# Kernel optimization log

Hardware: AMD Instinct MI355X
Metric: run time of the kernel (lower is better)

Reference implementation:

```python
import jax, jax.numpy as jnp
import numpy as np

TEMP = 0.07
K = 16  # n_hard_negatives
NEG = jnp.float32(-1e30)


def setup_inputs() -> dict:
    key = jax.random.key(0)
    k1, k2 = jax.random.split(key)
    B, D = 8192, 512
    emb = jax.random.normal(k1, (B, D), dtype=jnp.float32)
    emb = emb / jnp.linalg.norm(emb, axis=1, keepdims=True)  # module expects L2-normalized
    labels = jax.random.randint(k2, (B,), 0, 2048, dtype=jnp.int64)
    return {"embeddings": emb, "labels": labels}


def _masked_topk(sim, valid, k):
    # sim: [B,B] float, valid: [B,B] bool -> (top values [B,k], per-slot validity [B,k])
    masked = jnp.where(valid, sim, NEG)
    top = jax.lax.top_k(masked, k)[0]
    count = jnp.sum(valid, axis=1)
    kmask = jnp.arange(k)[None, :] < jnp.minimum(count, k)[:, None]
    return top, kmask


def reference(embeddings, labels):
    B = embeddings.shape[0]
    sim = embeddings @ embeddings.T                      # [B,B]
    same = labels[:, None] == labels[None, :]
    eye = jnp.eye(B, dtype=bool)
    pos_mask = same & ~eye                               # positives exclude self
    neg_mask = ~same                                     # diagonal is 'same', so self excluded

    pos_count = jnp.sum(pos_mask, axis=1)
    neg_count = jnp.sum(neg_mask, axis=1)
    row_valid = (pos_count > 0) & (neg_count > 0)

    # semi-hard: negatives with sim < min positive sim
    pos_min = jnp.min(jnp.where(pos_mask, sim, -NEG), axis=1)     # [B]
    semi = neg_mask & (sim < pos_min[:, None])
    has_semi = jnp.any(semi, axis=1)

    top_semi, m_semi = _masked_topk(sim, semi, K)
    top_all, m_all = _masked_topk(sim, neg_mask, K)
    top = jnp.where(has_semi[:, None], top_semi, top_all)         # [B,K]
    kmask = jnp.where(has_semi[:, None], m_semi, m_all)           # [B,K]

    pos_sim = jnp.sum(jnp.where(pos_mask, sim, 0.0), axis=1) / jnp.maximum(pos_count, 1) / TEMP

    # masked logsumexp over the (variable-length) top-k hard negatives
    scaled = jnp.where(kmask, top / TEMP, NEG)
    m = jnp.max(scaled, axis=1)
    sum_exp = jnp.sum(jnp.where(kmask, jnp.exp(scaled - m[:, None]), 0.0), axis=1)
    lse = m + jnp.log(jnp.maximum(sum_exp, 1e-30))

    loss_i = -pos_sim + lse
    n_valid = jnp.sum(row_valid)
    return jnp.sum(jnp.where(row_valid, loss_i, 0.0)) / jnp.maximum(n_valid, 1)
```

## Files before the change

### kernel.cpp

```cpp
#include <hip/hip_runtime.h>
#include <stdint.h>
#include <stddef.h>


#define TEMPV 0.07f
#define NEGV -1e30f

typedef short v8s __attribute__((ext_vector_type(8)));
typedef float v4f __attribute__((ext_vector_type(4)));

__device__ __forceinline__ short f2bf(float f) {
  unsigned u = __float_as_uint(f);
  unsigned r = (u + 0x7fffu + ((u >> 16) & 1u)) >> 16;
  return (short)r;
}
__device__ __forceinline__ float bf2f(short s) {
  return __uint_as_float(((unsigned)(unsigned short)s) << 16);
}

__device__ __forceinline__ void gload16(const void* g, void* l) {
  __builtin_amdgcn_global_load_lds((const __attribute__((address_space(1))) unsigned*)g,
                                   (__attribute__((address_space(3))) unsigned*)l, 16, 0, 0);
}

struct SNet { unsigned char a[64]; unsigned char b[64]; int n; };
constexpr SNet mknet16() {
  SNet t{}; t.n = 0;
  for (int p = 1; p < 16; p <<= 1)
    for (int k = p; k >= 1; k >>= 1)
      for (int j = k % p; j + k < 16; j += 2 * k)
        for (int i = 0; i < k; ++i) {
          int x = i + j, y = i + j + k;
          if (y < 16 && (x / (2 * p)) == (y / (2 * p))) {
            t.a[t.n] = (unsigned char)x; t.b[t.n] = (unsigned char)y; ++t.n;
          }
        }
  return t;
}
constexpr SNet NET16 = mknet16();
constexpr int NETN = NET16.n;

__device__ __forceinline__ void sort16d(float (&V)[16]) {
#pragma unroll
  for (int c = 0; c < NETN; ++c) {
    const int x = NET16.a[c], y = NET16.b[c];
    float hi = fmaxf(V[x], V[y]);
    float lo = fminf(V[x], V[y]);
    V[x] = hi; V[y] = lo;
  }
}

__device__ __forceinline__ void clean16d(float (&V)[16]) {
#pragma unroll
  for (int s = 8; s >= 1; s >>= 1) {
#pragma unroll
    for (int i = 0; i < 16; ++i) {
      if ((i & s) == 0) {
        float hi = fmaxf(V[i], V[i + s]);
        float lo = fminf(V[i], V[i + s]);
        V[i] = hi; V[i + s] = lo;
      }
    }
  }
}

__device__ __forceinline__ void mergeld(float (&R)[16], const float (&M)[16]) {
#pragma unroll
  for (int i = 0; i < 8; ++i) {
    float a = fmaxf(M[i], R[15 - i]);
    float b = fmaxf(M[15 - i], R[i]);
    R[i] = a; R[15 - i] = b;
  }
  clean16d(R);
}

__device__ __forceinline__ void xmerge16(float (&M)[16], int mask) {
#pragma unroll
  for (int i = 0; i < 8; ++i) {
    float pa = __shfl_xor(M[15 - i], mask);
    float pb = __shfl_xor(M[i], mask);
    M[i] = fmaxf(M[i], pa);
    M[15 - i] = fmaxf(M[15 - i], pb);
  }
  clean16d(M);
}

__device__ __forceinline__ void ins16(float (&L)[16], float v) {
#pragma unroll
  for (int k = 0; k < 15; ++k) {
    float lo = fminf(v, L[k + 1]);
    float hi = fmaxf(v, L[k + 1]);
    L[k] = lo;
    v = hi;
  }
  L[15] = v;
}

__global__ __launch_bounds__(256) void kconvh(const float* __restrict__ emb,
                                              short* __restrict__ emb16,
                                              const int* __restrict__ lab,
                                              int* __restrict__ hist,
                                              int* __restrict__ start,
                                              int* __restrict__ rows,
                                              float* lsum, int* nval, int* fbcnt) {
  __shared__ int h[2048];
  __shared__ int part[256];
  int t = threadIdx.x;
  if (blockIdx.x < 4096) {
    int i = (blockIdx.x * 256 + t) * 4;
    float4 v = *(const float4*)(emb + i);
    short4 s;
    s.x = f2bf(v.x); s.y = f2bf(v.y); s.z = f2bf(v.z); s.w = f2bf(v.w);
    *(short4*)(emb16 + i) = s;
    if (blockIdx.x == 0 && t == 0) { *lsum = 0.f; *nval = 0; *fbcnt = 0; }
    return;
  }
#pragma unroll
  for (int k = 0; k < 8; ++k) h[t * 8 + k] = 0;
  __syncthreads();
  for (int i = t; i < 8192; i += 256) atomicAdd(&h[lab[i]], 1);
  __syncthreads();
  int v[8], loc[8], s = 0;
#pragma unroll
  for (int k = 0; k < 8; ++k) v[k] = h[t * 8 + k];
#pragma unroll
  for (int k = 0; k < 8; ++k) { loc[k] = s; s += v[k]; }
  part[t] = s;
  __syncthreads();
  for (int off = 1; off < 256; off <<= 1) {
    int x = (t >= off) ? part[t - off] : 0;
    __syncthreads();
    part[t] += x;
    __syncthreads();
  }
  int base = (t > 0) ? part[t - 1] : 0;
#pragma unroll
  for (int k = 0; k < 8; ++k) {
    hist[t * 8 + k] = v[k];
    start[t * 8 + k] = base + loc[k];
  }
  __syncthreads();
#pragma unroll
  for (int k = 0; k < 8; ++k) h[t * 8 + k] = base + loc[k];
  __syncthreads();
  for (int i = t; i < 8192; i += 256) {
    int p = atomicAdd(&h[lab[i]], 1);
    rows[p] = i;
  }
}

__global__ __launch_bounds__(256) void kpos2(const short* __restrict__ emb16,
                                             const int* __restrict__ lab,
                                             const int* __restrict__ hist,
                                             const int* __restrict__ start,
                                             const int* __restrict__ rows,
                                             float* __restrict__ pmin,
                                             float* __restrict__ pterm,
                                             int* __restrict__ valid) {
  int t = threadIdx.x;
  int wv = t >> 6, lane = t & 63;
  int i = blockIdx.x * 4 + wv;
  int li = lab[i];
  int s0 = start[li], c = hist[li];
  float ei[8];
  v8s e = *(const v8s*)(emb16 + (size_t)i * 512 + lane * 8);
#pragma unroll
  for (int k = 0; k < 8; ++k) ei[k] = bf2f(e[k]);
  float smin = 1e30f, ssum = 0.f;
  for (int k = 0; k < c; ++k) {
    int j = rows[s0 + k];
    if (j == i) continue;
    v8s f = *(const v8s*)(emb16 + (size_t)j * 512 + lane * 8);
    float s = 0.f;
#pragma unroll
    for (int q = 0; q < 8; ++q) s += ei[q] * bf2f(f[q]);
#pragma unroll
    for (int off = 32; off; off >>= 1) s += __shfl_xor(s, off);
    smin = fminf(smin, s);
    ssum += s;
  }
  if (lane == 0) {
    int pc = c - 1, nc = 8192 - c;
    pmin[i] = smin;
    pterm[i] = ssum / (float)(pc > 0 ? pc : 1) / TEMPV;
    valid[i] = (pc > 0 && nc > 0) ? 1 : 0;
  }
}

__global__ __launch_bounds__(256, 2) void kgemm(const short* __restrict__ emb16,
                                                const int* __restrict__ lab,
                                                const float* __restrict__ pminA,
                                                float* __restrict__ Lsemi) {
  __shared__ __align__(16) short Cg[2][128][64];

  int t = threadIdx.x;
  int bid = blockIdx.x;
  int rb = bid >> 3, cb = bid & 7;
  int rowbase = rb * 64;
  int colblock = cb * 1024;

  int wv = t >> 6, l = t & 63;
  int l15 = l & 15, l4 = l >> 4;

  int myrow = rowbase + wv * 16 + l15;
  int rlab = lab[myrow];
  float pm = pminA[myrow];

  v8s brow[8][2];
#pragma unroll
  for (int kst = 0; kst < 8; ++kst)
#pragma unroll
    for (int h = 0; h < 2; ++h)
      brow[kst][h] =
          *(const v8s*)(emb16 + (size_t)myrow * 512 + kst * 64 + h * 32 + l4 * 8);

  float RS[16];
#pragma unroll
  for (int k = 0; k < 16; ++k) RS[k] = NEGV;

  v4f acc[8];
#pragma unroll
  for (int mi = 0; mi < 8; ++mi) acc[mi] = (v4f)0.f;

#pragma unroll
  for (int q = 0; q < 4; ++q) {
    int e = q * 256 + t;
    int col = e >> 3, ch = e & 7;
    gload16(emb16 + ((size_t)(colblock + col) * 512 + ((ch ^ (col & 7)) * 8)),
            &Cg[0][col][ch * 8]);
  }
  asm volatile("s_waitcnt vmcnt(0)" ::: "memory");
  __builtin_amdgcn_s_barrier();

  const int apos0 = (l4 ^ (l15 & 7)) * 8;

  for (int ct = 0; ct < 8; ++ct) {
#pragma unroll
    for (int kst = 0; kst < 8; ++kst) {
      const int cur = kst & 1;
      v8s a0[8], a1[8];
#pragma unroll
      for (int mi = 0; mi < 8; ++mi)
        a0[mi] = *(const v8s*)&Cg[cur][mi * 16 + l15][apos0];
#pragma unroll
      for (int mi = 0; mi < 8; ++mi)
        a1[mi] = *(const v8s*)&Cg[cur][mi * 16 + l15][apos0 ^ 32];
      if (!(ct == 7 && kst == 7)) {
        const int nct = (kst == 7) ? ct + 1 : ct;
        const int nk = ((kst + 1) & 7) * 64;
#pragma unroll
        for (int q = 0; q < 4; ++q) {
          int e = q * 256 + t;
          int col = e >> 3, ch = e & 7;
          gload16(emb16 + ((size_t)(colblock + nct * 128 + col) * 512 + nk +
                           ((ch ^ (col & 7)) * 8)),
                  &Cg[cur ^ 1][col][ch * 8]);
        }
      }
      __builtin_amdgcn_s_setprio(1);
#pragma unroll
      for (int mi = 0; mi < 8; ++mi)
        acc[mi] = __builtin_amdgcn_mfma_f32_16x16x32_bf16(a0[mi], brow[kst][0],
                                                          acc[mi], 0, 0, 0);
#pragma unroll
      for (int mi = 0; mi < 8; ++mi)
        acc[mi] = __builtin_amdgcn_mfma_f32_16x16x32_bf16(a1[mi], brow[kst][1],
                                                          acc[mi], 0, 0, 0);
      __builtin_amdgcn_s_setprio(0);
      if (kst == 7) {
        const int mycolbase = colblock + ct * 128;
#pragma unroll
        for (int c = 0; c < 2; ++c) {
          int lc[4][4];
#pragma unroll
          for (int mm = 0; mm < 4; ++mm) {
            int4 q = *(const int4*)&lab[mycolbase + (c * 4 + mm) * 16 + l4 * 4];
            lc[mm][0] = q.x; lc[mm][1] = q.y; lc[mm][2] = q.z; lc[mm][3] = q.w;
          }
          float S[16];
#pragma unroll
          for (int j = 0; j < 16; ++j) {
            const int mi = c * 4 + (j >> 2), r = j & 3;
            float v = acc[mi][r];
            bool keep = (lc[j >> 2][r] != rlab) && (v < pm);
            S[j] = keep ? v : NEGV;
          }
          sort16d(S);
          mergeld(RS, S);
        }
#pragma unroll
        for (int mi = 0; mi < 8; ++mi) acc[mi] = (v4f)0.f;
      }
      asm volatile("s_waitcnt vmcnt(0)" ::: "memory");
      __builtin_amdgcn_s_barrier();
    }
  }

  xmerge16(RS, 16);
  xmerge16(RS, 32);
  if (l4 == 0) {
    size_t o = ((size_t)cb * 8192 + myrow) * 16;
#pragma unroll
    for (int k = 0; k < 4; ++k)
      *(float4*)&Lsemi[o + k * 4] =
          make_float4(RS[k * 4], RS[k * 4 + 1], RS[k * 4 + 2], RS[k * 4 + 3]);
  }
}

__global__ __launch_bounds__(256) void kfin(const float* __restrict__ Lsemi,
                                            const float* __restrict__ pterm,
                                            const int* __restrict__ valid,
                                            float* lsum, int* nval,
                                            int* fbcnt, int* fbrows) {
  int i = blockIdx.x * 256 + threadIdx.x;
  float S[16], M[16];
#pragma unroll
  for (int k = 0; k < 16; ++k) S[k] = Lsemi[(size_t)i * 16 + k];
  for (int c = 1; c < 8; ++c) {
    size_t o = ((size_t)c * 8192 + i) * 16;
#pragma unroll
    for (int k = 0; k < 16; ++k) M[k] = Lsemi[o + k];
    mergeld(S, M);
  }
  int vd = valid[i];
  bool hs = S[0] > -1e29f;
  float li = 0.f;
  if (vd && !hs) {
    int idx = atomicAdd(fbcnt, 1);
    fbrows[idx] = i;
  } else if (vd) {
    float m = S[0] / TEMPV;
    float se = 0.f;
#pragma unroll
    for (int k = 0; k < 16; ++k)
      if (S[k] > -1e29f) se += expf(S[k] / TEMPV - m);
    li = m + logf(se) - pterm[i];
  }
#pragma unroll
  for (int off = 32; off; off >>= 1) {
    li += __shfl_xor(li, off);
    vd += __shfl_xor(vd, off);
  }
  __shared__ float rsd[4];
  __shared__ int rid[4];
  int wv = threadIdx.x >> 6;
  if ((threadIdx.x & 63) == 0) { rsd[wv] = li; rid[wv] = vd; }
  __syncthreads();
  if (threadIdx.x == 0) {
    atomicAdd(lsum, rsd[0] + rsd[1] + rsd[2] + rsd[3]);
    atomicAdd(nval, rid[0] + rid[1] + rid[2] + rid[3]);
  }
}

__global__ __launch_bounds__(256) void kfallA(const short* __restrict__ emb16,
                                              const int* __restrict__ lab,
                                              const int* __restrict__ fbcnt,
                                              const int* __restrict__ fbrows,
                                              float* __restrict__ fbpart) {
  int nfb = *fbcnt;
  if (nfb > 2048) nfb = 2048;
  int nunits = nfb * 32;
  __shared__ short remb[512];
  __shared__ float sims[256];
  int t = threadIdx.x;
  for (int u = blockIdx.x; u < nunits; u += gridDim.x) {
    int f = u >> 5, j = u & 31;
    int row = fbrows[f];
    int rl = lab[row];
    __syncthreads();
    if (t < 64) *(v8s*)&remb[t * 8] = *(const v8s*)(emb16 + (size_t)row * 512 + t * 8);
    __syncthreads();
    int c = j * 256 + t;
    float sz[8];
#pragma unroll
    for (int z = 0; z < 8; ++z) sz[z] = 0.f;
#pragma unroll 4
    for (int q = 0; q < 64; ++q) {
      v8s e = *(const v8s*)(emb16 + (size_t)c * 512 + q * 8);
      v8s r = *(const v8s*)&remb[q * 8];
#pragma unroll
      for (int z = 0; z < 8; ++z) sz[z] += bf2f(e[z]) * bf2f(r[z]);
    }
    float s = ((sz[0] + sz[1]) + (sz[2] + sz[3])) + ((sz[4] + sz[5]) + (sz[6] + sz[7]));
    sims[t] = (lab[c] != rl) ? s : NEGV;
    __syncthreads();
    if (t < 64) {
      float M[16];
#pragma unroll
      for (int k = 0; k < 16; ++k) M[k] = NEGV;
      M[0] = sims[t]; M[1] = sims[64 + t]; M[2] = sims[128 + t]; M[3] = sims[192 + t];
      sort16d(M);
      xmerge16(M, 1); xmerge16(M, 2); xmerge16(M, 4);
      xmerge16(M, 8); xmerge16(M, 16); xmerge16(M, 32);
      if (t == 0) {
#pragma unroll
        for (int k = 0; k < 16; ++k) fbpart[(size_t)(f * 32 + j) * 16 + k] = M[k];
      }
    }
  }
}

__global__ __launch_bounds__(256) void kout(const short* __restrict__ emb16,
                                            const int* __restrict__ lab,
                                            const int* __restrict__ fbcnt,
                                            const int* __restrict__ fbrows,
                                            const float* __restrict__ fbpart,
                                            const float* __restrict__ pterm,
                                            const float* lsum, const int* nval,
                                            float* out) {
  __shared__ float fsum[256];
  int t = threadIdx.x;
  int nfb = *fbcnt;
  float acc = 0.f;
  for (int f = t; f < nfb; f += 256) {
    int row = fbrows[f];
    float R[16];
    if (f < 2048) {
#pragma unroll
      for (int k = 0; k < 16; ++k) R[k] = fbpart[(size_t)(f * 32) * 16 + k];
      for (int j = 1; j < 32; ++j) {
        float M[16];
#pragma unroll
        for (int k = 0; k < 16; ++k) M[k] = fbpart[(size_t)(f * 32 + j) * 16 + k];
        mergeld(R, M);
      }
    } else {
      int rl = lab[row];
      float L[16];
#pragma unroll
      for (int k = 0; k < 16; ++k) L[k] = NEGV;
      for (int c = 0; c < 8192; ++c) {
        if (lab[c] == rl) continue;
        float s = 0.f;
        for (int q = 0; q < 64; ++q) {
          v8s e = *(const v8s*)(emb16 + (size_t)c * 512 + q * 8);
          v8s r = *(const v8s*)(emb16 + (size_t)row * 512 + q * 8);
#pragma unroll
          for (int z = 0; z < 8; ++z) s += bf2f(e[z]) * bf2f(r[z]);
        }
        if (s > L[0]) ins16(L, s);
      }
#pragma unroll
      for (int k = 0; k < 16; ++k) R[k] = L[15 - k];
    }
    float m = R[0] / TEMPV;
    float se = 0.f;
#pragma unroll
    for (int k = 0; k < 16; ++k)
      if (R[k] > -1e29f) se += expf(R[k] / TEMPV - m);
    acc += m + logf(se) - pterm[row];
  }
  fsum[t] = acc;
  __syncthreads();
  if (t == 0) {
    float s = *lsum;
    for (int k = 0; k < 256; ++k) s += fsum[k];
    int n = *nval;
    out[0] = s / (float)(n > 0 ? n : 1);
  }
}

extern "C" void kernel_launch(void* const* d_in, const int* in_sizes, int n_in,
                              void* d_out, int out_size, void* d_ws, size_t ws_size,
                              hipStream_t stream) {
  const float* emb = (const float*)d_in[0];
  const int* lab = (const int*)d_in[1];
  float* out = (float*)d_out;

  char* wsb = (char*)d_ws;
  short* emb16 = (short*)wsb;
  int* hist = (int*)(wsb + 8388608);
  int* start = (int*)(wsb + 8396800);
  int* rows = (int*)(wsb + 8404992);
  float* pmin = (float*)(wsb + 8437760);
  float* pterm = (float*)(wsb + 8470528);
  int* valid = (int*)(wsb + 8503296);
  float* LsemiW = (float*)(wsb + 8536064);
  int* fbcnt = (int*)(wsb + 12730368);
  int* fbrows = (int*)(wsb + 12730432);
  float* fbpart = (float*)(wsb + 12763200);
  float* lsum = (float*)(wsb + 16957504);
  int* nval = (int*)(wsb + 16957508);

  kconvh<<<4097, 256, 0, stream>>>(emb, emb16, lab, hist, start, rows, lsum, nval, fbcnt);
  kpos2<<<2048, 256, 0, stream>>>(emb16, lab, hist, start, rows, pmin, pterm, valid);
  kgemm<<<1024, 256, 0, stream>>>(emb16, lab, pmin, LsemiW);
  kfin<<<32, 256, 0, stream>>>(LsemiW, pterm, valid, lsum, nval, fbcnt, fbrows);
  kfallA<<<256, 256, 0, stream>>>(emb16, lab, fbcnt, fbrows, fbpart);
  kout<<<1, 256, 0, stream>>>(emb16, lab, fbcnt, fbrows, fbpart, pterm, lsum, nval, out);
}
```

Before: 174.1 us.

## Double K-slice per LDS stage and skip top-k merge when no candidate qualifies

Each LDS pipeline stage now covers 128 K-elements instead of 64. That halves the number of barriers and waitcnt stalls per column tile, and the XOR swizzle widens to 16 chunks. LDS use doubles to 64 KB per block, which may limit occupancy under launch_bounds(256,2). Separately, the sort-and-merge into the running top-16 is skipped when no lane in the wave has a candidate above its current 16th value. This saves sorting-network work once the list has filled, at the cost of an extra max reduction and a wave vote.

```diff
diff --git a/kernel.cpp b/kernel.cpp
--- a/kernel.cpp
+++ b/kernel.cpp
@@ -191,7 +191,7 @@
                                                 const int* __restrict__ lab,
                                                 const float* __restrict__ pminA,
                                                 float* __restrict__ Lsemi) {
-  __shared__ __align__(16) short Cg[2][128][64];
+  __shared__ __align__(16) short Cg[2][128][128];
 
   int t = threadIdx.x;
   int bid = blockIdx.x;
@@ -206,13 +206,10 @@
   int rlab = lab[myrow];
   float pm = pminA[myrow];
 
-  v8s brow[8][2];
-#pragma unroll
-  for (int kst = 0; kst < 8; ++kst)
-#pragma unroll
-    for (int h = 0; h < 2; ++h)
-      brow[kst][h] =
-          *(const v8s*)(emb16 + (size_t)myrow * 512 + kst * 64 + h * 32 + l4 * 8);
+  v8s brow[16];
+#pragma unroll
+  for (int ks = 0; ks < 16; ++ks)
+    brow[ks] = *(const v8s*)(emb16 + (size_t)myrow * 512 + ks * 32 + l4 * 8);
 
   float RS[16];
 #pragma unroll
@@ -222,52 +219,71 @@
 #pragma unroll
   for (int mi = 0; mi < 8; ++mi) acc[mi] = (v4f)0.f;
 
-#pragma unroll
-  for (int q = 0; q < 4; ++q) {
+  const int ap0 = ((0 | l4) ^ l15) * 8;
+  const int ap1 = ((4 | l4) ^ l15) * 8;
+  const int ap2 = ((8 | l4) ^ l15) * 8;
+  const int ap3 = ((12 | l4) ^ l15) * 8;
+
+#pragma unroll
+  for (int q = 0; q < 8; ++q) {
     int e = q * 256 + t;
-    int col = e >> 3, ch = e & 7;
-    gload16(emb16 + ((size_t)(colblock + col) * 512 + ((ch ^ (col & 7)) * 8)),
+    int col = e >> 4, ch = e & 15;
+    gload16(emb16 + ((size_t)(colblock + col) * 512 + ((ch ^ (col & 15)) * 8)),
             &Cg[0][col][ch * 8]);
   }
   asm volatile("s_waitcnt vmcnt(0)" ::: "memory");
   __builtin_amdgcn_s_barrier();
 
-  const int apos0 = (l4 ^ (l15 & 7)) * 8;
-
   for (int ct = 0; ct < 8; ++ct) {
 #pragma unroll
-    for (int kst = 0; kst < 8; ++kst) {
-      const int cur = kst & 1;
-      v8s a0[8], a1[8];
-#pragma unroll
-      for (int mi = 0; mi < 8; ++mi)
-        a0[mi] = *(const v8s*)&Cg[cur][mi * 16 + l15][apos0];
-#pragma unroll
-      for (int mi = 0; mi < 8; ++mi)
-        a1[mi] = *(const v8s*)&Cg[cur][mi * 16 + l15][apos0 ^ 32];
-      if (!(ct == 7 && kst == 7)) {
-        const int nct = (kst == 7) ? ct + 1 : ct;
-        const int nk = ((kst + 1) & 7) * 64;
-#pragma unroll
-        for (int q = 0; q < 4; ++q) {
+    for (int k4 = 0; k4 < 4; ++k4) {
+      const int cur = k4 & 1;
+      v8s a[8], b2[8];
+#pragma unroll
+      for (int mi = 0; mi < 8; ++mi)
+        a[mi] = *(const v8s*)&Cg[cur][mi * 16 + l15][ap0];
+#pragma unroll
+      for (int mi = 0; mi < 8; ++mi)
+        b2[mi] = *(const v8s*)&Cg[cur][mi * 16 + l15][ap1];
+      if (!(ct == 7 && k4 == 3)) {
+        const int nct = (k4 == 3) ? ct + 1 : ct;
+        const int nk = ((k4 + 1) & 3) * 128;
+#pragma unroll
+        for (int q = 0; q < 8; ++q) {
           int e = q * 256 + t;
-          int col = e >> 3, ch = e & 7;
+          int col = e >> 4, ch = e & 15;
           gload16(emb16 + ((size_t)(colblock + nct * 128 + col) * 512 + nk +
-                           ((ch ^ (col & 7)) * 8)),
+                           ((ch ^ (col & 15)) * 8)),
                   &Cg[cur ^ 1][col][ch * 8]);
         }
       }
       __builtin_amdgcn_s_setprio(1);
 #pragma unroll
       for (int mi = 0; mi < 8; ++mi)
-        acc[mi] = __builtin_amdgcn_mfma_f32_16x16x32_bf16(a0[mi], brow[kst][0],
+        acc[mi] = __builtin_amdgcn_mfma_f32_16x16x32_bf16(a[mi], brow[k4 * 4 + 0],
                                                           acc[mi], 0, 0, 0);
 #pragma unroll
       for (int mi = 0; mi < 8; ++mi)
-        acc[mi] = __builtin_amdgcn_mfma_f32_16x16x32_bf16(a1[mi], brow[kst][1],
+        acc[mi] = __builtin_amdgcn_mfma_f32_16x16x32_bf16(b2[mi], brow[k4 * 4 + 1],
                                                           acc[mi], 0, 0, 0);
       __builtin_amdgcn_s_setprio(0);
-      if (kst == 7) {
+#pragma unroll
+      for (int mi = 0; mi < 8; ++mi)
+        a[mi] = *(const v8s*)&Cg[cur][mi * 16 + l15][ap2];
+#pragma unroll
+      for (int mi = 0; mi < 8; ++mi)
+        b2[mi] = *(const v8s*)&Cg[cur][mi * 16 + l15][ap3];
+      __builtin_amdgcn_s_setprio(1);
+#pragma unroll
+      for (int mi = 0; mi < 8; ++mi)
+        acc[mi] = __builtin_amdgcn_mfma_f32_16x16x32_bf16(a[mi], brow[k4 * 4 + 2],
+                                                          acc[mi], 0, 0, 0);
+#pragma unroll
+      for (int mi = 0; mi < 8; ++mi)
+        acc[mi] = __builtin_amdgcn_mfma_f32_16x16x32_bf16(b2[mi], brow[k4 * 4 + 3],
+                                                          acc[mi], 0, 0, 0);
+      __builtin_amdgcn_s_setprio(0);
+      if (k4 == 3) {
         const int mycolbase = colblock + ct * 128;
 #pragma unroll
         for (int c = 0; c < 2; ++c) {
@@ -285,8 +301,13 @@
             bool keep = (lc[j >> 2][r] != rlab) && (v < pm);
             S[j] = keep ? v : NEGV;
           }
-          sort16d(S);
-          mergeld(RS, S);
+          float vm = S[0];
+#pragma unroll
+          for (int j = 1; j < 16; ++j) vm = fmaxf(vm, S[j]);
+          if (__any(vm > RS[15])) {
+            sort16d(S);
+            mergeld(RS, S);
+          }
         }
 #pragma unroll
         for (int mi = 0; mi < 8; ++mi) acc[mi] = (v4f)0.f;
```

Result: no change. 174.3 us (+0.1%).
